# Performance work log

Hardware: AMD Instinct MI355X
Metric: run time of the kernel (lower is better)

## Reference

```python
import jax, jax.numpy as jnp
import numpy as np

HS = 256      # hidden_size
HD = 256      # hidden_dim
B, L, S = 256, 400, 512
N = B * L
E = N * 4
NEG_SLOPE = 0.2


def setup_inputs() -> dict:
    key = jax.random.key(0)
    ks = iter(jax.random.split(key, 48))
    def rn(shape, scale=0.05):
        return jax.random.normal(next(ks), shape, jnp.float32) * scale
    inp = {}
    inp['emb'] = jax.random.normal(next(ks), (N, 640), jnp.float32)
    inp['x_tokens'] = jax.random.randint(next(ks), (N,), 0, 6, jnp.int32)
    inp['edge_src'] = jax.random.randint(next(ks), (E,), 0, N, jnp.int32)
    inp['edge_dst'] = jax.random.randint(next(ks), (E,), 0, N, jnp.int32)
    inp['batch_ids'] = (jnp.arange(N, dtype=jnp.int32) // L)
    inp['pos_ids'] = (jnp.arange(N, dtype=jnp.int32) % L)
    inp['mask'] = (jnp.arange(S)[None, :] < L).astype(jnp.float32) * jnp.ones((B, 1), jnp.float32)
    # parameters
    inp['emb_table'] = rn((6, HS))
    inp['W_e2g'] = rn((640, HS)); inp['b_e2g'] = jnp.zeros((HS,), jnp.float32)
    # GAT layers: (in, heads*out), att_src/att_dst [heads, out], bias [out]
    inp['W1'] = rn((HS, 4 * HD)); inp['asrc1'] = rn((4, HD)); inp['adst1'] = rn((4, HD)); inp['b1'] = jnp.zeros((HD,), jnp.float32)
    inp['W2'] = rn((HD, 4 * HD)); inp['asrc2'] = rn((4, HD)); inp['adst2'] = rn((4, HD)); inp['b2'] = jnp.zeros((HD,), jnp.float32)
    inp['W3'] = rn((HD, 1 * HS)); inp['asrc3'] = rn((1, HS)); inp['adst3'] = rn((1, HS)); inp['b3'] = jnp.zeros((HS,), jnp.float32)
    inp['W_le'] = rn((640, HS)); inp['b_le'] = jnp.zeros((HS,), jnp.float32)
    # CNN conv kernels: OIH layout [out=128, in=256, k]
    inp['k7'] = rn((HS // 2, HS, 7)); inp['cb7'] = jnp.zeros((HS // 2,), jnp.float32)
    inp['k11'] = rn((HS // 2, HS, 11)); inp['cb11'] = jnp.zeros((HS // 2,), jnp.float32)
    inp['k15'] = rn((HS // 2, HS, 15)); inp['cb15'] = jnp.zeros((HS // 2,), jnp.float32)
    inp['Wl1'] = rn((HS // 2, 512)); inp['bl1'] = jnp.zeros((512,), jnp.float32)
    inp['Wl2'] = rn((512, HS)); inp['bl2'] = jnp.zeros((HS,), jnp.float32)
    return inp


def _gat(x, src, dst, W, a_src, a_dst, b, heads, out_dim):
    # PyG GATConv, concat=False, eval (no dropout), with self-loops.
    n = x.shape[0]
    h = (x @ W).reshape(n, heads, out_dim)             # [N,H,C]
    al_s = (h * a_src[None]).sum(-1)                   # [N,H]
    al_d = (h * a_dst[None]).sum(-1)                   # [N,H]
    e = al_s[src] + al_d[dst]                          # [E,H]
    e = jnp.where(e > 0, e, NEG_SLOPE * e)             # leaky_relu(0.2)
    m = jax.ops.segment_max(e, dst, num_segments=n)
    m = jnp.where(jnp.isfinite(m), m, 0.0)
    ex = jnp.exp(e - m[dst])
    denom = jax.ops.segment_sum(ex, dst, num_segments=n) + 1e-16
    alpha = ex / denom[dst]                            # [E,H]
    out = jax.ops.segment_sum(alpha[:, :, None] * h[src], dst, num_segments=n)
    return out.mean(axis=1) + b                        # concat=False -> mean over heads


def _conv1d(x, w, b, pad):
    # x: [B,C,S], w: [O,I,k]
    y = jax.lax.conv_general_dilated(x, w, (1,), [(pad, pad)],
                                     dimension_numbers=('NCH', 'OIH', 'NCH'))
    return y + b[None, :, None]


def reference(emb, x_tokens, edge_src, edge_dst, batch_ids, pos_ids, mask,
              emb_table, W_e2g, b_e2g,
              W1, asrc1, adst1, b1, W2, asrc2, adst2, b2, W3, asrc3, adst3, b3,
              W_le, b_le, k7, cb7, k11, cb11, k15, cb15, Wl1, bl1, Wl2, bl2):
    n = emb.shape[0]
    # self-loops (PyG GATConv default)
    loops = jnp.arange(n, dtype=edge_src.dtype)
    src = jnp.concatenate([edge_src, loops])
    dst = jnp.concatenate([edge_dst, loops])

    x_r = emb_table[x_tokens]                          # [N,HS]
    x_g = jax.nn.relu(emb @ W_e2g + b_e2g)             # [N,HS]
    x = jax.nn.relu(_gat(x_g, src, dst, W1, asrc1, adst1, b1, 4, HD))
    x = jax.nn.relu(_gat(x, src, dst, W2, asrc2, adst2, b2, 4, HD))
    x = jax.nn.relu(_gat(x, src, dst, W3, asrc3, adst3, b3, 1, HS))

    emb_l = jax.nn.relu(emb @ W_le + b_le)             # [N,HS]

    # ragged -> padded [B,S,HS] via scatter (vectorized form of the python loop)
    zeros = jnp.zeros((mask.shape[0], S, HS), jnp.float32)
    out_r = zeros.at[batch_ids, pos_ids].set((x_r + emb_l) / 2)

    # CNN (eval: dropout = identity)
    xc = out_r.transpose(0, 2, 1)                      # [B,HS,S]
    x1 = _conv1d(xc, k7, cb7, 3)
    x2 = _conv1d(xc, k11, cb11, 5)
    x3 = _conv1d(xc, k15, cb15, 7)
    xc = ((x1 + x2 + x3) / 3).transpose(0, 2, 1)       # [B,S,128]
    xc = jax.nn.relu(xc @ Wl1 + bl1) @ Wl2 + bl2       # [B,S,HS]

    emb_seq = (xc * mask[:, :, None]).mean(axis=1)     # [B,HS]
    return emb_seq
```

## Files before the change

### kernel.cpp

```cpp
#include <hip/hip_runtime.h>

#define NNODES 102400
#define NBATCH 256
#define LSEQ   400
#define SPAD   416
#define HS     256
#define KDIM   640
#define OC     128
#define NTAP   15
#define H1     512
#define STILE  80
#define SROWS  94

typedef __attribute__((ext_vector_type(8))) short short8;
typedef __attribute__((ext_vector_type(4))) float floatx4;

__device__ inline unsigned short f2bf(float f) {
    unsigned u = __builtin_bit_cast(unsigned, f);
    unsigned r = (u + 0x7FFFu + ((u >> 16) & 1u)) >> 16;
    return (unsigned short)r;
}

__device__ inline void gld_lds16(const void* g, void* l) {
    __builtin_amdgcn_global_load_lds(
        (const __attribute__((address_space(1))) unsigned int*)g,
        (__attribute__((address_space(3))) unsigned int*)l, 16, 0, 0);
}

__global__ __launch_bounds__(256) void setup_all(
    const float* __restrict__ k7, const float* __restrict__ k11,
    const float* __restrict__ k15, const float* __restrict__ cb7,
    const float* __restrict__ cb11, const float* __restrict__ cb15,
    const float* __restrict__ W_le, const float* __restrict__ Wl1,
    unsigned short* __restrict__ Wpk, float* __restrict__ bc,
    unsigned short* __restrict__ Wle_pk, unsigned short* __restrict__ Wl1_pk,
    unsigned short* __restrict__ seq, float* __restrict__ A_acc)
{
    int bid = blockIdx.x, tid = threadIdx.x;
    if (bid < 512) {
        int idx = bid * 256 + tid;
        int b = idx >> 9, within = idx & 511;
        int rowi = within >> 5, c = within & 31;
        int srow = rowi < 8 ? rowi : 400 + rowi;
        ((uint4*)seq)[((size_t)b * SPAD + srow) * 32 + c] = make_uint4(0u, 0u, 0u, 0u);
    } else if (bid < 2432) {
        int idx = (bid - 512) * 256 + tid;
        int oc = idx & (OC - 1);
        int ic = (idx >> 7) & (HS - 1);
        int d  = idx / (OC * HS);
        float wv = k15[(oc * HS + ic) * 15 + d];
        int t11 = d - 2;
        if (t11 >= 0 && t11 < 11) wv += k11[(oc * HS + ic) * 11 + t11];
        int t7 = d - 4;
        if (t7 >= 0 && t7 < 7)   wv += k7[(oc * HS + ic) * 7 + t7];
        wv *= (1.0f / 3.0f);
        int kc = ic >> 6, ks = (ic >> 5) & 1, qq = (ic >> 3) & 3, j = ic & 7;
        int nt = oc >> 4, n = oc & 15;
        int pidx = ((((d * 4 + kc) * 2 + ks) * 8 + nt) * 64 + (qq * 16 + n)) * 8 + j;
        Wpk[pidx] = f2bf(wv);
        if (idx < OC) bc[idx] = (cb7[idx] + cb11[idx] + cb15[idx]) * (1.0f / 3.0f);
    } else if (bid < 3072) {
        int idx = (bid - 2432) * 256 + tid;
        int k = idx >> 8, col = idx & 255;
        int t = k >> 6, ks = (k >> 5) & 1, qq = (k >> 3) & 3, j = k & 7;
        int nt = col >> 4, n = col & 15;
        int pidx = (((t * 2 + ks) * 16 + nt) * 64 + (qq * 16 + n)) * 8 + j;
        Wle_pk[pidx] = f2bf(W_le[k * 256 + col]);
    } else if (bid < 3328) {
        int idx = (bid - 3072) * 256 + tid;
        int k = idx >> 9, col = idx & 511;
        int ks = k >> 5, qq = (k >> 3) & 3, j = k & 7;
        int jbb = col >> 7, nhnt = (col >> 4) & 7, n = col & 15;
        int pidx = jbb * 16384 + ((ks * 8 + nhnt) * 64 + (qq * 16 + n)) * 8 + j;
        Wl1_pk[pidx] = f2bf(Wl1[k * 512 + col]);
    } else {
        int idx = (bid - 3328) * 256 + tid;
        ((float4*)A_acc)[idx] = make_float4(0.f, 0.f, 0.f, 0.f);
    }
}

union GemmSm {
    struct { unsigned short As[64][72]; unsigned short Bsh[16384]; } s;
    unsigned short Cs[64][264];
};

__global__ __launch_bounds__(512, 4) void gemm_emb(
    const float* __restrict__ emb, const int* __restrict__ x_tokens,
    const float* __restrict__ emb_table,
    const unsigned short* __restrict__ Wle_pk, const float* __restrict__ b_le,
    unsigned short* __restrict__ seq)
{
    __shared__ __align__(16) GemmSm g;
    int row0 = blockIdx.x * 64;
    int tid = threadIdx.x;
    int w = tid >> 6, lane = tid & 63;
    int q = lane >> 4, m = lane & 15;
    int mh = w >> 2, nh = w & 3;

    int ar = tid >> 3;
    int ac = (tid & 7) * 8;

    floatx4 acc[2][4] = {};
    const uint4* wp = (const uint4*)Wle_pk;

    for (int t = 0; t < 10; t++) {
        __syncthreads();
        {
            const float4* src = (const float4*)&emb[(size_t)(row0 + ar) * KDIM + t * 64 + ac];
            #pragma unroll
            for (int u = 0; u < 2; u++) {
                float4 f = src[u];
                ushort4 h;
                h.x = f2bf(f.x); h.y = f2bf(f.y); h.z = f2bf(f.z); h.w = f2bf(f.w);
                *(ushort4*)&g.s.As[ar][ac + u * 4] = h;
            }
        }
        #pragma unroll
        for (int i = 0; i < 4; i++) {
            gld_lds16(wp + (size_t)t * 2048 + i * 512 + tid,
                      &g.s.Bsh[(size_t)(i * 512 + w * 64) * 8]);
        }
        __syncthreads();

        #pragma unroll
        for (int ks = 0; ks < 2; ks++) {
            short8 a0 = *(const short8*)&g.s.As[mh * 32 +  0 + m][ks * 32 + q * 8];
            short8 a1 = *(const short8*)&g.s.As[mh * 32 + 16 + m][ks * 32 + q * 8];
            #pragma unroll
            for (int nt = 0; nt < 4; nt++) {
                short8 bf = *(const short8*)&g.s.Bsh[(size_t)((ks * 16 + nh * 4 + nt) * 64 + lane) * 8];
                acc[0][nt] = __builtin_amdgcn_mfma_f32_16x16x32_bf16(a0, bf, acc[0][nt], 0, 0, 0);
                acc[1][nt] = __builtin_amdgcn_mfma_f32_16x16x32_bf16(a1, bf, acc[1][nt], 0, 0, 0);
            }
        }
    }

    __syncthreads();
    #pragma unroll
    for (int nt = 0; nt < 4; nt++) {
        int col = nh * 64 + nt * 16 + m;
        float blv = b_le[col];
        #pragma unroll
        for (int mt = 0; mt < 2; mt++) {
            #pragma unroll
            for (int r = 0; r < 4; r++) {
                int row = mh * 32 + mt * 16 + q * 4 + r;
                int tok = x_tokens[row0 + row];
                float v = acc[mt][nt][r] + blv;
                v = v > 0.f ? v : 0.f;
                g.Cs[row][col] = f2bf(0.5f * (v + emb_table[tok * HS + col]));
            }
        }
    }
    __syncthreads();
    #pragma unroll
    for (int rr = 0; rr < 8; rr++) {
        int node = row0 + w * 8 + rr;
        int b = node / LSEQ;
        int p = node - b * LSEQ;
        ushort4 val = *(const ushort4*)&g.Cs[w * 8 + rr][lane * 4];
        *(ushort4*)&seq[((size_t)b * SPAD + (p + 8)) * HS + lane * 4] = val;
    }
}

union ConvSm {
    unsigned short As[SROWS][264];
    struct {
        float red[40 * 132];
        unsigned short abf[STILE][136];
    } p2;
};

__device__ __forceinline__ void conv_load_Bh(
    const short8* __restrict__ wb, int h, int kh, int nh, int lane, short8 bf[4])
{
    int c = h >> 1, ks = h & 1;
    int d = c >> 1, kc = kh * 2 + (c & 1);
    const short8* bp = wb + (size_t)(d * 4 + kc) * 1024 + nh * 256 + ks * 512 + lane;
    #pragma unroll
    for (int nt = 0; nt < 4; nt++)
        bf[nt] = bp[nt * 64];
}

__device__ __forceinline__ void conv_mfma_half(
    const unsigned short (*As)[264], floatx4 acc[5][4],
    const short8 bf[4], int h, int kh, int m, int q)
{
    int c = h >> 1, ks = h & 1;
    int d = c >> 1, kc = kh * 2 + (c & 1);
    #pragma unroll
    for (int mt = 0; mt < 5; mt++) {
        short8 a = *(const short8*)&As[mt * 16 + m + d][kc * 64 + ks * 32 + q * 8];
        #pragma unroll
        for (int nt = 0; nt < 4; nt++)
            acc[mt][nt] = __builtin_amdgcn_mfma_f32_16x16x32_bf16(a, bf[nt], acc[mt][nt], 0, 0, 0);
    }
}

__global__ __launch_bounds__(256, 3) void conv_fused(
    const unsigned short* __restrict__ seq, const unsigned short* __restrict__ Wpk,
    const float* __restrict__ bc, const unsigned short* __restrict__ Wl1_pk,
    const float* __restrict__ bl1, float* __restrict__ A_acc)
{
    __shared__ __align__(16) ConvSm sm;

    int b  = blockIdx.y;
    int s0 = blockIdx.x * STILE;
    int tid = threadIdx.x;
    int w = tid >> 6, lane = tid & 63;
    int q = lane >> 4, m = lane & 15;
    int nh = w >> 1, kh = w & 1;

    const short8* wb = (const short8*)Wpk;
    short8 bA[4], bB[4];
    conv_load_Bh(wb, 0, kh, nh, lane, bA);

    {
        const uint4* sp = (const uint4*)(seq + ((size_t)b * SPAD + s0 + 1) * HS);
        #pragma unroll
        for (int pass = 0; pass < 12; pass++) {
            int idx = pass * 256 + tid;
            if (idx < SROWS * 32) {
                int r = idx >> 5, c = idx & 31;
                *(uint4*)&sm.As[r][c * 8] = sp[r * 32 + c];
            }
        }
    }
    __syncthreads();

    floatx4 acc[5][4] = {};

    for (int h = 0; h < 60; h += 2) {
        conv_load_Bh(wb, h + 1, kh, nh, lane, bB);
        conv_mfma_half(sm.As, acc, bA, h, kh, m, q);
        if (h + 2 < 60) conv_load_Bh(wb, h + 2, kh, nh, lane, bA);
        conv_mfma_half(sm.As, acc, bB, h + 1, kh, m, q);
    }

    float bc0 = bc[lane * 2], bc1 = bc[lane * 2 + 1];
    __syncthreads();
    #pragma unroll
    for (int hh = 0; hh < 2; hh++) {
        if (kh == 1) {
            #pragma unroll
            for (int mt = 0; mt < 5; mt++)
                #pragma unroll
                for (int nt = 0; nt < 4; nt++)
                    #pragma unroll
                    for (int r = 0; r < 4; r++) {
                        int row = mt * 16 + q * 4 + r;
                        if (row >= hh * 40 && row < hh * 40 + 40)
                            sm.p2.red[(row - hh * 40) * 132 + nh * 64 + nt * 16 + m] = acc[mt][nt][r];
                    }
        }
        __syncthreads();
        if (kh == 0) {
            #pragma unroll
            for (int mt = 0; mt < 5; mt++)
                #pragma unroll
                for (int nt = 0; nt < 4; nt++)
                    #pragma unroll
                    for (int r = 0; r < 4; r++) {
                        int row = mt * 16 + q * 4 + r;
                        if (row >= hh * 40 && row < hh * 40 + 40)
                            sm.p2.red[(row - hh * 40) * 132 + nh * 64 + nt * 16 + m] += acc[mt][nt][r];
                    }
        }
        __syncthreads();
        #pragma unroll
        for (int rr = 0; rr < 10; rr++) {
            int lrow = w * 10 + rr;
            float2 v = *(const float2*)&sm.p2.red[lrow * 132 + lane * 2];
            unsigned uo = (unsigned)f2bf(v.x + bc0) | ((unsigned)f2bf(v.y + bc1) << 16);
            *(unsigned*)&sm.p2.abf[hh * 40 + lrow][lane * 2] = uo;
        }
        __syncthreads();
    }

    const short8* wl1 = (const short8*)Wl1_pk;
    short8 f0[8], f1[8];
    #pragma unroll
    for (int ks = 0; ks < 4; ks++)
        #pragma unroll
        for (int nt = 0; nt < 2; nt++)
            f0[ks * 2 + nt] = wl1[(ks * 8 + w * 2 + nt) * 64 + lane];
    #pragma unroll
    for (int ks = 0; ks < 4; ks++)
        #pragma unroll
        for (int nt = 0; nt < 2; nt++)
            f1[ks * 2 + nt] = wl1[2048 + (ks * 8 + w * 2 + nt) * 64 + lane];

    #pragma unroll
    for (int jb = 0; jb < 4; jb++) {
        floatx4 acc2[5][2] = {};
        const short8* fcur = (jb & 1) ? f1 : f0;
        #pragma unroll
        for (int ks = 0; ks < 4; ks++) {
            short8 bf0 = fcur[ks * 2 + 0];
            short8 bf1 = fcur[ks * 2 + 1];
            #pragma unroll
            for (int mt = 0; mt < 5; mt++) {
                short8 a = *(const short8*)&sm.p2.abf[mt * 16 + m][ks * 32 + q * 8];
                acc2[mt][0] = __builtin_amdgcn_mfma_f32_16x16x32_bf16(a, bf0, acc2[mt][0], 0, 0, 0);
                acc2[mt][1] = __builtin_amdgcn_mfma_f32_16x16x32_bf16(a, bf1, acc2[mt][1], 0, 0, 0);
            }
        }
        if (jb < 2) {
            short8* fnext = (jb & 1) ? f1 : f0;
            #pragma unroll
            for (int ks = 0; ks < 4; ks++)
                #pragma unroll
                for (int nt = 0; nt < 2; nt++)
                    fnext[ks * 2 + nt] = wl1[(size_t)(jb + 2) * 2048 + (ks * 8 + w * 2 + nt) * 64 + lane];
        }
        #pragma unroll
        for (int nt = 0; nt < 2; nt++) {
            int j = jb * 128 + w * 32 + nt * 16 + m;
            float blv = bl1[j];
            float vsum = 0.f;
            #pragma unroll
            for (int mt = 0; mt < 5; mt++)
                #pragma unroll
                for (int r = 0; r < 4; r++) {
                    float v = acc2[mt][nt][r] + blv;
                    vsum += v > 0.f ? v : 0.f;
                }
            vsum += __shfl_xor(vsum, 16, 64);
            vsum += __shfl_xor(vsum, 32, 64);
            if (q == 0) atomicAdd(&A_acc[(size_t)b * H1 + j], vsum);
        }
    }
}

__global__ __launch_bounds__(256) void final_out(
    const float* __restrict__ A_acc, const float* __restrict__ Wl2,
    const float* __restrict__ bl2, float* __restrict__ out)
{
    __shared__ float a[H1];
    int b = blockIdx.x, tid = threadIdx.x;
    a[tid] = A_acc[(size_t)b * H1 + tid];
    a[tid + 256] = A_acc[(size_t)b * H1 + tid + 256];
    __syncthreads();
    float acc = 0.f;
    #pragma unroll 8
    for (int k = 0; k < H1; k++)
        acc += a[k] * Wl2[(size_t)k * HS + tid];
    out[(size_t)b * HS + tid] = acc * (1.0f / 512.0f) + bl2[tid] * (400.0f / 512.0f);
}

extern "C" void kernel_launch(void* const* d_in, const int* in_sizes, int n_in,
                              void* d_out, int out_size, void* d_ws, size_t ws_size,
                              hipStream_t stream)
{
    const float* emb       = (const float*)d_in[0];
    const int*   x_tokens  = (const int*)d_in[1];
    const float* emb_table = (const float*)d_in[7];
    const float* W_le = (const float*)d_in[22];
    const float* b_le = (const float*)d_in[23];
    const float* k7   = (const float*)d_in[24];
    const float* cb7  = (const float*)d_in[25];
    const float* k11  = (const float*)d_in[26];
    const float* cb11 = (const float*)d_in[27];
    const float* k15  = (const float*)d_in[28];
    const float* cb15 = (const float*)d_in[29];
    const float* Wl1  = (const float*)d_in[30];
    const float* bl1  = (const float*)d_in[31];
    const float* Wl2  = (const float*)d_in[32];
    const float* bl2  = (const float*)d_in[33];
    float* out = (float*)d_out;

    char* p = (char*)d_ws;
    unsigned short* seqb = (unsigned short*)p;       p += (size_t)NBATCH * SPAD * HS * 2;
    unsigned short* Wpk = (unsigned short*)p;        p += (size_t)NTAP * HS * OC * 2;
    unsigned short* Wle_pk = (unsigned short*)p;     p += (size_t)KDIM * HS * 2;
    unsigned short* Wl1_pk = (unsigned short*)p;     p += (size_t)OC * H1 * 2;
    float* bcv = (float*)p;                          p += 512;
    float* A_acc = (float*)p;                        p += (size_t)NBATCH * H1 * 4;

    setup_all<<<dim3(3456), 256, 0, stream>>>(
        k7, k11, k15, cb7, cb11, cb15, W_le, Wl1,
        Wpk, bcv, Wle_pk, Wl1_pk, seqb, A_acc);
    gemm_emb<<<dim3(NNODES / 64), 512, 0, stream>>>(
        emb, x_tokens, emb_table, Wle_pk, b_le, seqb);
    conv_fused<<<dim3(5, NBATCH), 256, 0, stream>>>(
        seqb, Wpk, bcv, Wl1_pk, bl1, A_acc);
    final_out<<<NBATCH, 256, 0, stream>>>(A_acc, Wl2, bl2, out);
}
```

Measured before the change: 577.3 us.

## Restructure embedding GEMM with register-prefetched double-buffered A and direct B loads

The emb@W_le GEMM kernel drops from 512 to 256 threads. Each wave now computes a 64x64 tile with 4x4 accumulators. B fragments are read straight from global memory into registers instead of being staged through LDS. The A tile is double-buffered in LDS, with the next K-slice prefetched into registers while the current MFMAs run, and it uses one barrier per step instead of two. This aims to hide global load latency and cut LDS traffic and syncs, at the cost of more registers (launch bounds lowered to 3 blocks) and repeated per-wave global B reads.

```diff
diff --git a/kernel.cpp b/kernel.cpp
--- a/kernel.cpp
+++ b/kernel.cpp
@@ -80,11 +80,11 @@
 }
 
 union GemmSm {
-    struct { unsigned short As[64][72]; unsigned short Bsh[16384]; } s;
+    unsigned short As[2][64][72];
     unsigned short Cs[64][264];
 };
 
-__global__ __launch_bounds__(512, 4) void gemm_emb(
+__global__ __launch_bounds__(256, 3) void gemm_emb(
     const float* __restrict__ emb, const int* __restrict__ x_tokens,
     const float* __restrict__ emb_table,
     const unsigned short* __restrict__ Wle_pk, const float* __restrict__ b_le,
@@ -95,56 +95,106 @@
     int tid = threadIdx.x;
     int w = tid >> 6, lane = tid & 63;
     int q = lane >> 4, m = lane & 15;
-    int mh = w >> 2, nh = w & 3;
-
-    int ar = tid >> 3;
-    int ac = (tid & 7) * 8;
-
-    floatx4 acc[2][4] = {};
-    const uint4* wp = (const uint4*)Wle_pk;
-
-    for (int t = 0; t < 10; t++) {
-        __syncthreads();
+
+    int ar = tid >> 2;
+    int ac = (tid & 3) * 16;
+
+    const short8* wle = (const short8*)Wle_pk;
+    const float4* arow = (const float4*)&emb[(size_t)(row0 + ar) * KDIM + ac];
+
+    float4 aregA[4], aregB[4];
+    #pragma unroll
+    for (int u = 0; u < 4; u++) aregA[u] = arow[u];
+    #pragma unroll
+    for (int u = 0; u < 4; u++) aregB[u] = arow[16 + u];
+    #pragma unroll
+    for (int u = 0; u < 4; u++) {
+        float4 f = aregA[u];
+        ushort4 h; h.x = f2bf(f.x); h.y = f2bf(f.y); h.z = f2bf(f.z); h.w = f2bf(f.w);
+        *(ushort4*)&g.As[0][ar][ac + u * 4] = h;
+    }
+    asm volatile("s_waitcnt lgkmcnt(0)" ::: "memory");
+    __builtin_amdgcn_s_barrier();
+
+    floatx4 acc[4][4] = {};
+    for (int tt = 0; tt < 10; tt += 2) {
         {
-            const float4* src = (const float4*)&emb[(size_t)(row0 + ar) * KDIM + t * 64 + ac];
-            #pragma unroll
-            for (int u = 0; u < 2; u++) {
-                float4 f = src[u];
-                ushort4 h;
-                h.x = f2bf(f.x); h.y = f2bf(f.y); h.z = f2bf(f.z); h.w = f2bf(f.w);
-                *(ushort4*)&g.s.As[ar][ac + u * 4] = h;
-            }
-        }
-        #pragma unroll
-        for (int i = 0; i < 4; i++) {
-            gld_lds16(wp + (size_t)t * 2048 + i * 512 + tid,
-                      &g.s.Bsh[(size_t)(i * 512 + w * 64) * 8]);
-        }
-        __syncthreads();
-
-        #pragma unroll
-        for (int ks = 0; ks < 2; ks++) {
-            short8 a0 = *(const short8*)&g.s.As[mh * 32 +  0 + m][ks * 32 + q * 8];
-            short8 a1 = *(const short8*)&g.s.As[mh * 32 + 16 + m][ks * 32 + q * 8];
-            #pragma unroll
-            for (int nt = 0; nt < 4; nt++) {
-                short8 bf = *(const short8*)&g.s.Bsh[(size_t)((ks * 16 + nh * 4 + nt) * 64 + lane) * 8];
-                acc[0][nt] = __builtin_amdgcn_mfma_f32_16x16x32_bf16(a0, bf, acc[0][nt], 0, 0, 0);
-                acc[1][nt] = __builtin_amdgcn_mfma_f32_16x16x32_bf16(a1, bf, acc[1][nt], 0, 0, 0);
-            }
-        }
-    }
-
-    __syncthreads();
+            const int t = tt;
+            short8 bf[8];
+            #pragma unroll
+            for (int ks = 0; ks < 2; ks++)
+                #pragma unroll
+                for (int nt = 0; nt < 4; nt++)
+                    bf[ks * 4 + nt] = wle[(size_t)t * 2048 + ks * 1024 + (w * 4 + nt) * 64 + lane];
+            if (t + 2 < 10) {
+                #pragma unroll
+                for (int u = 0; u < 4; u++) aregA[u] = arow[(t + 2) * 16 + u];
+            }
+            #pragma unroll
+            for (int ks = 0; ks < 2; ks++) {
+                #pragma unroll
+                for (int mt = 0; mt < 4; mt++) {
+                    short8 a = *(const short8*)&g.As[0][mt * 16 + m][ks * 32 + q * 8];
+                    #pragma unroll
+                    for (int nt = 0; nt < 4; nt++)
+                        acc[mt][nt] = __builtin_amdgcn_mfma_f32_16x16x32_bf16(a, bf[ks * 4 + nt], acc[mt][nt], 0, 0, 0);
+                }
+            }
+            if (t + 1 < 10) {
+                #pragma unroll
+                for (int u = 0; u < 4; u++) {
+                    float4 f = aregB[u];
+                    ushort4 h; h.x = f2bf(f.x); h.y = f2bf(f.y); h.z = f2bf(f.z); h.w = f2bf(f.w);
+                    *(ushort4*)&g.As[1][ar][ac + u * 4] = h;
+                }
+            }
+            asm volatile("s_waitcnt lgkmcnt(0)" ::: "memory");
+            __builtin_amdgcn_s_barrier();
+        }
+        {
+            const int t = tt + 1;
+            short8 bf[8];
+            #pragma unroll
+            for (int ks = 0; ks < 2; ks++)
+                #pragma unroll
+                for (int nt = 0; nt < 4; nt++)
+                    bf[ks * 4 + nt] = wle[(size_t)t * 2048 + ks * 1024 + (w * 4 + nt) * 64 + lane];
+            if (t + 2 < 10) {
+                #pragma unroll
+                for (int u = 0; u < 4; u++) aregB[u] = arow[(t + 2) * 16 + u];
+            }
+            #pragma unroll
+            for (int ks = 0; ks < 2; ks++) {
+                #pragma unroll
+                for (int mt = 0; mt < 4; mt++) {
+                    short8 a = *(const short8*)&g.As[1][mt * 16 + m][ks * 32 + q * 8];
+                    #pragma unroll
+                    for (int nt = 0; nt < 4; nt++)
+                        acc[mt][nt] = __builtin_amdgcn_mfma_f32_16x16x32_bf16(a, bf[ks * 4 + nt], acc[mt][nt], 0, 0, 0);
+                }
+            }
+            if (t + 1 < 10) {
+                #pragma unroll
+                for (int u = 0; u < 4; u++) {
+                    float4 f = aregA[u];
+                    ushort4 h; h.x = f2bf(f.x); h.y = f2bf(f.y); h.z = f2bf(f.z); h.w = f2bf(f.w);
+                    *(ushort4*)&g.As[0][ar][ac + u * 4] = h;
+                }
+            }
+            asm volatile("s_waitcnt lgkmcnt(0)" ::: "memory");
+            __builtin_amdgcn_s_barrier();
+        }
+    }
+
     #pragma unroll
     for (int nt = 0; nt < 4; nt++) {
-        int col = nh * 64 + nt * 16 + m;
+        int col = w * 64 + nt * 16 + m;
         float blv = b_le[col];
         #pragma unroll
-        for (int mt = 0; mt < 2; mt++) {
+        for (int mt = 0; mt < 4; mt++) {
             #pragma unroll
             for (int r = 0; r < 4; r++) {
-                int row = mh * 32 + mt * 16 + q * 4 + r;
+                int row = mt * 16 + q * 4 + r;
                 int tok = x_tokens[row0 + row];
                 float v = acc[mt][nt][r] + blv;
                 v = v > 0.f ? v : 0.f;
@@ -152,13 +202,14 @@
             }
         }
     }
-    __syncthreads();
-    #pragma unroll
-    for (int rr = 0; rr < 8; rr++) {
-        int node = row0 + w * 8 + rr;
+    asm volatile("s_waitcnt lgkmcnt(0)" ::: "memory");
+    __builtin_amdgcn_s_barrier();
+    #pragma unroll
+    for (int rr = 0; rr < 16; rr++) {
+        int node = row0 + w * 16 + rr;
         int b = node / LSEQ;
         int p = node - b * LSEQ;
-        ushort4 val = *(const ushort4*)&g.Cs[w * 8 + rr][lane * 4];
+        ushort4 val = *(const ushort4*)&g.Cs[w * 16 + rr][lane * 4];
         *(ushort4*)&seq[((size_t)b * SPAD + (p + 8)) * HS + lane * 4] = val;
     }
 }
@@ -380,7 +431,7 @@
     setup_all<<<dim3(3456), 256, 0, stream>>>(
         k7, k11, k15, cb7, cb11, cb15, W_le, Wl1,
         Wpk, bcv, Wle_pk, Wl1_pk, seqb, A_acc);
-    gemm_emb<<<dim3(NNODES / 64), 512, 0, stream>>>(
+    gemm_emb<<<dim3(NNODES / 64), 256, 0, stream>>>(
         emb, x_tokens, emb_table, Wle_pk, b_le, seqb);
     conv_fused<<<dim3(5, NBATCH), 256, 0, stream>>>(
         seqb, Wpk, bcv, Wl1_pk, bl1, A_acc);
```

Result: no change. 578.8 us (+0.3%).
